# Kernel optimization log

Measured on AMD Instinct MI355X. Metric: run time of the kernel, lower is better.

Reference implementation:

```python
import jax, jax.numpy as jnp
import numpy as np

B, L, D, C, NL = 32, 512, 768, 97, 2  # batch, seq_len, hidden, class_nums, gat_layers


def setup_inputs() -> dict:
    key = jax.random.key(0)
    ks = jax.random.split(key, 16)

    def n(k, shape, scale=0.02):
        return jax.random.normal(k, shape, dtype=jnp.float32) * scale

    return dict(
        x=n(ks[0], (B, L, D), 1.0),                 # encoder output
        pos1=jnp.ones((B, L), jnp.float32),          # entity-1 position mask
        pos2=jnp.ones((B, L), jnp.float32),          # entity-2 position mask
        mask=jnp.ones((B, L), jnp.int32),            # attention mask (1 = keep)
        emb=n(ks[1], (C, D), 1.0),                   # relation label embedding table
        rel_w=n(ks[2], (D, D)), rel_b=jnp.zeros((D,), jnp.float32),
        # per-layer, per-RA (axis1: 0=ra1, 1=ra2) parameters
        qw=n(ks[3], (NL, 2, D, D)), qb=jnp.zeros((NL, 2, D), jnp.float32),
        kw=n(ks[4], (NL, 2, D, D)), kb=jnp.zeros((NL, 2, D), jnp.float32),
        vw=n(ks[5], (NL, 2, D, D)), vb=jnp.zeros((NL, 2, D), jnp.float32),
        sw=n(ks[6], (NL, 2, 2 * D)), sb=jnp.zeros((NL, 2), jnp.float32),   # score: Linear(2d,1)
        gw=n(ks[7], (NL, 2, 2 * D)), gb=jnp.zeros((NL, 2), jnp.float32),   # gate:  Linear(2d,1)
        fc1_w=n(ks[8], (3 * D, D)), fc1_b=jnp.zeros((D,), jnp.float32),
        fc2_w=n(ks[9], (D,)), fc2_b=jnp.zeros((), jnp.float32),
    )


def _relation_attention(p, x, qw, qb, kw, kb, vw, vb, sw, sb, gw, gb, mask):
    # p: (b, c, d) queries; x: (b, l, d) keys/values
    d = p.shape[-1]
    q = jnp.einsum('bcd,de->bce', p, qw) + qb          # (b, c, d)
    k = jnp.einsum('bld,de->ble', x, kw) + kb          # (b, l, d)
    # score = Linear(concat([q_i, k_j])) is separable: q@sw[:d] + k@sw[d:] + sb
    score = (q @ sw[:d])[:, :, None] + (k @ sw[d:])[:, None, :] + sb  # (b, c, l)
    if mask is not None:
        score = jnp.where(mask[:, None, :] == 0, jnp.float32(-1e9), score)
    attn = jax.nn.softmax(score, axis=2)
    v = jnp.einsum('bld,de->ble', x, vw) + vb          # (b, l, d)
    out = jnp.einsum('bcl,bld->bcd', attn, v) + p      # (b, c, d)
    # gate = sigmoid(Linear(concat([out, p]))), also separable
    g = jax.nn.sigmoid(out @ gw[:d] + p @ gw[d:] + gb)[..., None]
    return g * out + (1.0 - g) * p


def reference(x, pos1, pos2, mask, emb, rel_w, rel_b,
              qw, qb, kw, kb, vw, vb, sw, sb, gw, gb,
              fc1_w, fc1_b, fc2_w, fc2_b):
    b, d = x.shape[0], x.shape[-1]
    # p = relation(embedding(arange(C))) broadcast over batch
    p = emb @ rel_w + rel_b                            # (C, d)
    p = jnp.broadcast_to(p[None], (b,) + p.shape)      # (b, C, d)

    for li in range(qw.shape[0]):
        x = _relation_attention(x, p, qw[li, 0], qb[li, 0], kw[li, 0], kb[li, 0],
                                vw[li, 0], vb[li, 0], sw[li, 0], sb[li, 0],
                                gw[li, 0], gb[li, 0], None) + x
        p = _relation_attention(p, x, qw[li, 1], qb[li, 1], kw[li, 1], kb[li, 1],
                                vw[li, 1], vb[li, 1], sw[li, 1], sb[li, 1],
                                gw[li, 1], gb[li, 1], mask) + p

    def pool_avg(pos):
        return jnp.sum(x * pos[:, :, None], axis=1) / jnp.sum(pos, axis=1)[:, None]

    e1 = pool_avg(pos1)                                # (b, d)
    e2 = pool_avg(pos2)                                # (b, d)
    cshape = p.shape                                   # (b, C, d)
    pc = jnp.concatenate([p,
                          jnp.broadcast_to(e1[:, None, :], cshape),
                          jnp.broadcast_to(e2[:, None, :], cshape)], axis=2)  # (b, C, 3d)
    h = jnp.tanh(pc @ fc1_w + fc1_b)                   # (b, C, d)
    logits = jax.nn.sigmoid(h @ fc2_w + fc2_b)         # (b, C)
    pred = jnp.argmax(logits, axis=1)                  # (b,)
    return logits, pred
```

## Files before the change

### kernel.cpp

```cpp
#include <hip/hip_runtime.h>
#include <math.h>

#define NBLK 512
#define NTHR 256
static const int Bb = 32, Ls = 512, Dd = 768, Cc = 97;

struct KArgs {
    const float *x0, *pos1, *pos2;
    const int* mask;
    const float *emb, *rel_w, *rel_b, *kw, *vw, *vb, *sw, *gw, *gb;
    const float *fc1w, *fc1b, *fc2w, *fc2b;
    float* out;
    float *p0b, *pp, *sc, *avx1, *avx2, *av1, *av2, *aw1, *aw2, *S0, *S1, *xp1, *xp2, *geb;
    float *kvecs, *pdots, *g1buf, *xd, *gx1, *gx2, *awb;
    float* zbase;
    int zcount;
};

__device__ __forceinline__ float sigm(float x) { return 1.f / (1.f + expf(-x)); }

__device__ __forceinline__ float wred(float v) {
#pragma unroll
    for (int o = 32; o > 0; o >>= 1) v += __shfl_down(v, o, 64);
    return v;
}

__device__ __forceinline__ float blk_sum4(float v, float* shr) {
    v = wred(v);
    int t = threadIdx.x;
    if ((t & 63) == 0) shr[t >> 6] = v;
    __syncthreads();
    float r = shr[0] + shr[1] + shr[2] + shr[3];
    __syncthreads();
    return r;
}

__device__ void sgemm_dev(const float* __restrict__ A, const float* __restrict__ W,
                          const float* __restrict__ bias, float* __restrict__ C,
                          int M, int N, int K, int KC, int bx, int by, int bz,
                          float* As, float* Ws) {
    int tid = threadIdx.x;
    int tx = tid & 15, ty = tid >> 4;
    int bn = bx * 64, bm = by * 64;
    int kb = bz * KC;
    int arow = tid >> 2, akq = (tid & 3) << 2;
    int wrow = tid >> 4, wcol = (tid & 15) << 2;
    int gar = bm + arow;
    bool aval = gar < M;
    const float* Ap = A + (size_t)gar * K + kb + akq;
    const float* Wp = W + (size_t)(kb + wrow) * N + bn + wcol;
    float acc[4][4] = {{0.f}};
    float4 a4 = make_float4(0.f, 0.f, 0.f, 0.f);
    if (aval) a4 = *(const float4*)Ap;
    float4 w4 = *(const float4*)Wp;
    for (int k0 = 0; k0 < KC; k0 += 16) {
        __syncthreads();
        As[(akq + 0) * 64 + arow] = a4.x; As[(akq + 1) * 64 + arow] = a4.y;
        As[(akq + 2) * 64 + arow] = a4.z; As[(akq + 3) * 64 + arow] = a4.w;
        *(float4*)&Ws[wrow * 64 + wcol] = w4;
        __syncthreads();
        if (k0 + 16 < KC) {
            if (aval) a4 = *(const float4*)(Ap + k0 + 16);
            w4 = *(const float4*)(Wp + (size_t)(k0 + 16) * N);
        }
#pragma unroll
        for (int kk = 0; kk < 16; ++kk) {
            float4 a = *(const float4*)&As[kk * 64 + (ty << 2)];
            float4 b = *(const float4*)&Ws[kk * 64 + (tx << 2)];
            acc[0][0]+=a.x*b.x; acc[0][1]+=a.x*b.y; acc[0][2]+=a.x*b.z; acc[0][3]+=a.x*b.w;
            acc[1][0]+=a.y*b.x; acc[1][1]+=a.y*b.y; acc[1][2]+=a.y*b.z; acc[1][3]+=a.y*b.w;
            acc[2][0]+=a.z*b.x; acc[2][1]+=a.z*b.y; acc[2][2]+=a.z*b.z; acc[2][3]+=a.z*b.w;
            acc[3][0]+=a.w*b.x; acc[3][1]+=a.w*b.y; acc[3][2]+=a.w*b.z; acc[3][3]+=a.w*b.w;
        }
    }
    int gc = bn + (tx << 2);
    float4 bz4 = make_float4(0.f, 0.f, 0.f, 0.f);
    if (bz == 0 && bias) bz4 = *(const float4*)(bias + gc);
#pragma unroll
    for (int i = 0; i < 4; ++i) {
        int gr = bm + (ty << 2) + i;
        if (gr < M) {
            float* cp = C + (size_t)gr * N + gc;
            atomicAdd(cp + 0, acc[i][0] + bz4.x); atomicAdd(cp + 1, acc[i][1] + bz4.y);
            atomicAdd(cp + 2, acc[i][2] + bz4.z); atomicAdd(cp + 3, acc[i][3] + bz4.w);
        }
    }
}

__device__ void attn_gemv(const KArgs& a, int phase, int jlin,
                          float* xs, float* lw, float* shr) {
    int t = threadIdx.x;
    int jt = jlin % 3, b = (jlin / 3) % 32, kseg = jlin / 96;
    float v = -3.0e38f, g1 = 0.f;
    if (t < Cc) {
        if (phase == 0) v = a.pdots[t];
        else {
            g1 = sigm(a.pdots[194 + t] + a.sc[128 + b] + a.gb[1]);
            v = 2.f * a.pdots[97 + t] + g1 * a.sc[160 + b];
        }
    }
    if (phase == 1 && jt == 0 && kseg == 0 && t < Cc) a.g1buf[(size_t)b * Cc + t] = g1;
    float m = v;
#pragma unroll
    for (int o = 32; o > 0; o >>= 1) m = fmaxf(m, __shfl_down(m, o, 64));
    if ((t & 63) == 0) shr[t >> 6] = m;
    __syncthreads();
    m = fmaxf(fmaxf(shr[0], shr[1]), fmaxf(shr[2], shr[3]));
    __syncthreads();
    float e = (t < Cc) ? expf(v - m) : 0.f;
    float s = blk_sum4(e, shr);
    float wc = e / s;
    if (t < Cc) lw[t] = wc;
    float cg1 = blk_sum4(wc * g1, shr);
    float alpha = (phase == 0) ? 1.f : 2.f;
    if (t < 96) {
        int d = kseg * 96 + t;
        const float* pc = a.p0b + d;
        float acc2 = 0.f;
#pragma unroll 4
        for (int c = 0; c < Cc; ++c) acc2 += lw[c] * pc[(size_t)c * Dd];
        float val = alpha * acc2;
        if (phase == 1) val += cg1 * a.av1[(size_t)b * Dd + d];
        xs[t] = val;
    }
    __syncthreads();
    const float* W = a.vw + (size_t)(phase == 0 ? 0 : 2) * Dd * Dd;
    const float* bias = a.vb + (phase == 0 ? 0 : 2) * Dd;
    float* outp = (phase == 0) ? a.avx1 : a.avx2;
    int j = jt * 256 + t;
    float acc = (kseg == 0) ? bias[j] : 0.f;
    const float* wp = W + (size_t)(kseg * 96) * Dd + j;
#pragma unroll 8
    for (int dd = 0; dd < 96; ++dd) acc += xs[dd] * wp[(size_t)dd * Dd];
    atomicAdd(&outp[(size_t)b * Dd + j], acc);
    const float* da[4]; const float* db[4]; int nd; float* dout;
    if (phase == 0) {
        da[0]=a.gw;          db[0]=nullptr;
        da[1]=a.kvecs+Dd;    db[1]=nullptr;
        da[2]=a.gw+3072;     db[2]=a.gw+3840;
        da[3]=a.kvecs+3*Dd;  db[3]=nullptr;
        nd = 4; dout = a.sc;
    } else {
        da[0]=a.gw+3072;     db[0]=nullptr;
        da[1]=a.kvecs+3*Dd;  db[1]=nullptr;
        nd = 2; dout = a.sc + 224;
    }
    for (int vv = 0; vv < nd; ++vv) {
        float wv = da[vv][j] + (db[vv] ? db[vv][j] : 0.f);
        float p = blk_sum4(acc * wv, shr);
        if (t == 0) atomicAdd(&dout[vv * 32 + b], p);
    }
}

__device__ void mm_dev(const KArgs& a, int jlin, const float* S, float gamma,
                       const float* avA, const float* coefA, float multA,
                       const float* avB, const float* coefB, float multB,
                       const float* W, const float* bias, float* outp,
                       int ndots, const float* d0a, const float* d0b,
                       const float* d1a, const float* d2a, const float* d2b,
                       float* dout, float* xs, float* shr) {
    int t = threadIdx.x;
    int jt = jlin % 3, b = (jlin / 3) % 32, kseg = jlin / 96;
    if (t < 96) {
        int d = kseg * 96 + t;
        float v = gamma * S[(size_t)b * Dd + d];
        if (avA) v += multA * coefA[b] * avA[(size_t)b * Dd + d];
        if (avB) v += multB * coefB[b] * avB[(size_t)b * Dd + d];
        xs[t] = v;
    }
    __syncthreads();
    int j = jt * 256 + t;
    float acc = (kseg == 0 && bias) ? bias[j] : 0.f;
    const float* wp = W + (size_t)(kseg * 96) * Dd + j;
#pragma unroll 8
    for (int dd = 0; dd < 96; ++dd) acc += xs[dd] * wp[(size_t)dd * Dd];
    atomicAdd(&outp[(size_t)b * Dd + j], acc);
    if (ndots > 0) {
        float wv = d0a[j] + (d0b ? d0b[j] : 0.f);
        float p = blk_sum4(acc * wv, shr);
        if (t == 0) atomicAdd(&dout[b], p);
    }
    if (ndots > 1) {
        float p = blk_sum4(acc * d1a[j], shr);
        if (t == 0) atomicAdd(&dout[32 + b], p);
    }
    if (ndots > 2) {
        float wv = d2a[j] + (d2b ? d2b[j] : 0.f);
        float p = blk_sum4(acc * wv, shr);
        if (t == 0) atomicAdd(&dout[64 + b], p);
    }
}

__device__ void ge_dev(const KArgs& a, int jlin, float* xs, float* xs2) {
    int t = threadIdx.x;
    int jt = jlin % 3, b = (jlin / 3) % 32, kseg = jlin / 96;
    if (t < 96) {
        int d = kseg * 96 + t;
        float a1 = a.avx1[(size_t)b * Dd + d], a2 = a.avx2[(size_t)b * Dd + d];
        xs[t]  = (4.f * a.xp1[(size_t)b * Dd + d] + 2.f * a.sc[448 + b] * a1 + a.sc[480 + b] * a2) * a.sc[576 + b];
        xs2[t] = (4.f * a.xp2[(size_t)b * Dd + d] + 2.f * a.sc[512 + b] * a1 + a.sc[544 + b] * a2) * a.sc[608 + b];
    }
    __syncthreads();
    int j = jt * 256 + t;
    float a1 = 0.f, a2 = 0.f;
    const float* w1 = a.fc1w + (size_t)(Dd + kseg * 96) * Dd + j;
    const float* w2 = a.fc1w + (size_t)(2 * Dd + kseg * 96) * Dd + j;
#pragma unroll 8
    for (int dd = 0; dd < 96; ++dd) {
        a1 += xs[dd] * w1[(size_t)dd * Dd];
        a2 += xs2[dd] * w2[(size_t)dd * Dd];
    }
    float res = a1 + a2 + (kseg == 0 ? a.fc1b[j] : 0.f);
    atomicAdd(&a.geb[(size_t)b * Dd + j], res);
}

__device__ void aw_dual_dev(const KArgs& a, int jlin, float* xs, float* xs2) {
    int t = threadIdx.x;
    int jt = jlin % 3, b = (jlin / 3) % 32, kseg = jlin / 96;
    if (t < 96) {
        int d = kseg * 96 + t;
        xs[t]  = a.av1[(size_t)b * Dd + d];
        xs2[t] = a.av2[(size_t)b * Dd + d];
    }
    __syncthreads();
    int j = jt * 256 + t;
    float a1 = 0.f, a2 = 0.f;
    const float* wp = a.fc1w + (size_t)(kseg * 96) * Dd + j;
#pragma unroll 8
    for (int dd = 0; dd < 96; ++dd) {
        float w = wp[(size_t)dd * Dd];
        a1 += xs[dd] * w;
        a2 += xs2[dd] * w;
    }
    atomicAdd(&a.aw1[(size_t)b * Dd + j], a1);
    atomicAdd(&a.aw2[(size_t)b * Dd + j], a2);
}

__device__ void softgate_dev(const KArgs& a, int phase, int b, float* shr) {
    int t = threadIdx.x;
    float ks[2], ga[2] = {0.f, 0.f}, gb2[2] = {0.f, 0.f};
#pragma unroll
    for (int i = 0; i < 2; ++i) {
        int l = t + (i << 8);
        size_t r = (size_t)b * Ls + l;
        float4 x = *(const float4*)(a.xd + r * 4);
        if (phase == 0) {
            float g = sigm(x.x + a.sc[b] + a.gb[0]);
            a.gx1[r] = g;
            ga[i] = g;
            ks[i] = 2.f * x.y + g * a.sc[32 + b];
        } else {
            float gp = a.gx1[r];
            float g = sigm(2.f * x.z + gp * a.sc[64 + b] + a.sc[224 + b] + a.gb[2]);
            a.gx2[r] = g;
            ga[i] = gp; gb2[i] = g;
            ks[i] = 4.f * x.w + 2.f * gp * a.sc[96 + b] + g * a.sc[256 + b];
        }
        if (a.mask[r] == 0) ks[i] = -1e9f;
    }
    float mx = fmaxf(ks[0], ks[1]);
#pragma unroll
    for (int o = 32; o > 0; o >>= 1) mx = fmaxf(mx, __shfl_down(mx, o, 64));
    if ((t & 63) == 0) shr[t >> 6] = mx;
    __syncthreads();
    mx = fmaxf(fmaxf(shr[0], shr[1]), fmaxf(shr[2], shr[3]));
    __syncthreads();
    float e0 = expf(ks[0] - mx), e1 = expf(ks[1] - mx);
    float s = blk_sum4(e0 + e1, shr);
    float inv = 1.f / s;
    float w0 = e0 * inv, w1 = e1 * inv;
    a.awb[(size_t)b * Ls + t] = w0;
    a.awb[(size_t)b * Ls + t + 256] = w1;
    float ca = blk_sum4(w0 * ga[0] + w1 * ga[1], shr);
    if (phase == 0) {
        if (t == 0) a.sc[320 + b] = ca;
    } else {
        if (t == 0) a.sc[352 + b] = ca;
        float cb = blk_sum4(w0 * gb2[0] + w1 * gb2[1], shr);
        if (t == 0) a.sc[384 + b] = cb;
        float q1a = a.pos1[(size_t)b * Ls + t], q1b = a.pos1[(size_t)b * Ls + t + 256];
        float q2a = a.pos2[(size_t)b * Ls + t], q2b = a.pos2[(size_t)b * Ls + t + 256];
        float s1 = blk_sum4(q1a + q1b, shr);
        float s2 = blk_sum4(q2a + q2b, shr);
        float c11 = blk_sum4(q1a * ga[0] + q1b * ga[1], shr);
        float c12 = blk_sum4(q1a * gb2[0] + q1b * gb2[1], shr);
        float c21 = blk_sum4(q2a * ga[0] + q2b * ga[1], shr);
        float c22 = blk_sum4(q2a * gb2[0] + q2b * gb2[1], shr);
        if (t == 0) {
            a.sc[448 + b] = c11; a.sc[480 + b] = c12;
            a.sc[512 + b] = c21; a.sc[544 + b] = c22;
            a.sc[576 + b] = 1.f / s1; a.sc[608 + b] = 1.f / s2;
        }
    }
}

__device__ void passX_dev(const KArgs& a, int blk, float* S, bool dopos) {
    int t = threadIdx.x;
    if (t >= 192) return;
    int b = blk >> 4, seg = blk & 15, l0 = seg * 32;
    int d4 = t << 2;
    const float* xb = a.x0 + ((size_t)b * Ls + l0) * Dd + d4;
    const float* wb = a.awb + (size_t)b * Ls + l0;
    float4 as = make_float4(0.f,0.f,0.f,0.f);
    float4 a1 = make_float4(0.f,0.f,0.f,0.f);
    float4 a2 = make_float4(0.f,0.f,0.f,0.f);
    for (int l = 0; l < 32; ++l) {
        float4 xv = *(const float4*)(xb + (size_t)l * Dd);
        float wv = wb[l];
        as.x += wv*xv.x; as.y += wv*xv.y; as.z += wv*xv.z; as.w += wv*xv.w;
        if (dopos) {
            float q1 = a.pos1[(size_t)b * Ls + l0 + l], q2 = a.pos2[(size_t)b * Ls + l0 + l];
            a1.x += q1*xv.x; a1.y += q1*xv.y; a1.z += q1*xv.z; a1.w += q1*xv.w;
            a2.x += q2*xv.x; a2.y += q2*xv.y; a2.z += q2*xv.z; a2.w += q2*xv.w;
        }
    }
    float* ds = S + (size_t)b * Dd + d4;
    atomicAdd(ds+0, as.x); atomicAdd(ds+1, as.y); atomicAdd(ds+2, as.z); atomicAdd(ds+3, as.w);
    if (dopos) {
        float* d1 = a.xp1 + (size_t)b * Dd + d4;
        float* d2 = a.xp2 + (size_t)b * Dd + d4;
        atomicAdd(d1+0, a1.x); atomicAdd(d1+1, a1.y); atomicAdd(d1+2, a1.z); atomicAdd(d1+3, a1.w);
        atomicAdd(d2+0, a2.x); atomicAdd(d2+1, a2.y); atomicAdd(d2+2, a2.z); atomicAdd(d2+3, a2.w);
    }
}

__global__ __launch_bounds__(NTHR) void k_zero_kvec(KArgs a) {
    int blk = blockIdx.x, t = threadIdx.x;
    int wv_ = t >> 6, lane = t & 63;
    for (size_t i = (size_t)blk * NTHR + t; i < (size_t)a.zcount; i += (size_t)NBLK * NTHR)
        a.zbase[i] = 0.f;
    int g = blk * 4 + wv_;
    for (int rep = 0; rep < 2; ++rep) {
        int dot = g + rep * 2048;
        if (dot < 3072) {
            int idx = dot / Dd, d = dot - idx * Dd;
            const float* row = a.kw + ((size_t)idx * Dd + d) * Dd;
            const float* swk = a.sw + (size_t)idx * 2 * Dd + Dd;
            float sA = 0.f;
            for (int j = lane; j < Dd; j += 64) sA += row[j] * swk[j];
            sA = wred(sA);
            if (lane == 0) a.kvecs[dot] = sA;
        }
    }
}

__global__ __launch_bounds__(NTHR) void k_gemm1(KArgs a) {
    __shared__ float As[1024], Ws[1024];
    int blk = blockIdx.x;
    sgemm_dev(a.emb, a.rel_w, a.rel_b, a.p0b, Cc, Dd, Dd, 96,
              blk % 12, (blk / 12) % 2, blk / 24, As, Ws);
}

__global__ __launch_bounds__(NTHR) void k_prep2(KArgs a) {
    __shared__ float As[1024], Ws[1024];
    int blk = blockIdx.x, t = threadIdx.x;
    int wv_ = t >> 6, lane = t & 63;
    if (blk < 96) {
        sgemm_dev(a.p0b, a.fc1w, nullptr, a.pp, Cc, Dd, Dd, 192,
                  blk % 12, (blk / 12) % 2, blk / 24, As, Ws);
    } else if (blk < 128) {
        int g2 = (blk - 96) * 4 + wv_;
        for (int k = 0; k < 4; ++k) {
            int j = g2 + k * 128;
            if (k == 3) { if (g2 >= 4) break; j = 384 + g2; }
            if (j >= 388) continue;
            int vv = j / Cc, r = j - vv * Cc;
            const float* va; const float* vb2 = nullptr;
            if (vv == 0) va = a.kvecs;
            else if (vv == 1) va = a.kvecs + 2 * Dd;
            else if (vv == 2) { va = a.gw + 1536; vb2 = a.gw + 2304; }
            else { va = a.gw + 4608; vb2 = a.gw + 5376; }
            const float* row = a.p0b + (size_t)r * Dd;
            float sA = 0.f;
            for (int jj = lane; jj < Dd; jj += 64)
                sA += row[jj] * (va[jj] + (vb2 ? vb2[jj] : 0.f));
            sA = wred(sA);
            if (lane == 0) a.pdots[j] = sA;
        }
    } else {
        float4 gs0[3], k1r[3], gs2[3], k3r[3];
#pragma unroll
        for (int k = 0; k < 3; ++k) {
            int d = (lane << 2) + k * 256;
            float4 ga = *(const float4*)(a.gw + d);
            float4 gbv = *(const float4*)(a.gw + 768 + d);
            gs0[k] = make_float4(ga.x+gbv.x, ga.y+gbv.y, ga.z+gbv.z, ga.w+gbv.w);
            k1r[k] = *(const float4*)(a.kvecs + 768 + d);
            float4 g2a = *(const float4*)(a.gw + 3072 + d);
            float4 g2b = *(const float4*)(a.gw + 3840 + d);
            gs2[k] = make_float4(g2a.x+g2b.x, g2a.y+g2b.y, g2a.z+g2b.z, g2a.w+g2b.w);
            k3r[k] = *(const float4*)(a.kvecs + 2304 + d);
        }
        int gwv = (blk - 128) * 4 + wv_;
        for (int r = gwv; r < Bb * Ls; r += 1536) {
            const float* xr = a.x0 + (size_t)r * Dd;
            float s0 = 0.f, s1 = 0.f, s2 = 0.f, s3 = 0.f;
#pragma unroll
            for (int k = 0; k < 3; ++k) {
                float4 xv = *(const float4*)(xr + (lane << 2) + k * 256);
                s0 += xv.x*gs0[k].x + xv.y*gs0[k].y + xv.z*gs0[k].z + xv.w*gs0[k].w;
                s1 += xv.x*k1r[k].x + xv.y*k1r[k].y + xv.z*k1r[k].z + xv.w*k1r[k].w;
                s2 += xv.x*gs2[k].x + xv.y*gs2[k].y + xv.z*gs2[k].z + xv.w*gs2[k].w;
                s3 += xv.x*k3r[k].x + xv.y*k3r[k].y + xv.z*k3r[k].z + xv.w*k3r[k].w;
            }
            s0 = wred(s0); s1 = wred(s1); s2 = wred(s2); s3 = wred(s3);
            if (lane == 0) {
                float4 o4 = make_float4(s0, s1, s2, s3);
                *(float4*)(a.xd + (size_t)r * 4) = o4;
            }
        }
    }
}

__global__ __launch_bounds__(NTHR) void k_attn(KArgs a, int phase) {
    __shared__ float xs[96], lw[128], shr[16];
    attn_gemv(a, phase, blockIdx.x, xs, lw, shr);
}

__global__ __launch_bounds__(NTHR) void k_softgate(KArgs a, int phase) {
    __shared__ float shr[16];
    softgate_dev(a, phase, blockIdx.x, shr);
}

__global__ __launch_bounds__(NTHR) void k_passX0(KArgs a) {
    passX_dev(a, blockIdx.x, a.S0, true);
}

__global__ __launch_bounds__(NTHR) void k_mm0(KArgs a) {
    __shared__ float xs[96], shr[16];
    mm_dev(a, blockIdx.x, a.S0, 2.f, a.avx1, a.sc + 320, 1.f, nullptr, nullptr, 0.f,
           a.vw + (size_t)1 * Dd * Dd, a.vb + Dd, a.av1,
           3, a.gw + 1536, nullptr, a.kvecs + 2 * Dd, a.gw + 4608, a.gw + 5376,
           a.sc + 128, xs, shr);
}

__global__ __launch_bounds__(NTHR) void k_passX1ge(KArgs a) {
    __shared__ float xs[96], xs2[96];
    int blk = blockIdx.x;
    if (blk < 512) passX_dev(a, blk, a.S1, false);
    else ge_dev(a, blk - 512, xs, xs2);
}

__global__ __launch_bounds__(NTHR) void k_mm1(KArgs a) {
    __shared__ float xs[96], shr[16];
    mm_dev(a, blockIdx.x, a.S1, 4.f, a.avx1, a.sc + 352, 2.f, a.avx2, a.sc + 384, 1.f,
           a.vw + (size_t)3 * Dd * Dd, a.vb + 3 * Dd, a.av2,
           1, a.gw + 4608, nullptr, nullptr, nullptr, nullptr,
           a.sc + 288, xs, shr);
}

__global__ __launch_bounds__(NTHR) void k_awdual(KArgs a) {
    __shared__ float xs[96], xs2[96];
    aw_dual_dev(a, blockIdx.x, xs, xs2);
}

__global__ __launch_bounds__(NTHR) void k_logits(KArgs a) {
    __shared__ float shr[16];
    int blk = blockIdx.x, t = threadIdx.x;
    for (int r = blk; r < Bb * Cc; r += NBLK) {
        int b = r / Cc, c = r - b * Cc;
        float g1 = a.g1buf[r];
        float g2 = sigm(2.f * a.pdots[291 + c] + g1 * a.sc[192 + b] + a.sc[288 + b] + a.gb[3]);
        float ssum = 0.f;
#pragma unroll
        for (int sseg = 0; sseg < 3; ++sseg) {
            int d = t + sseg * 256;
            float h = tanhf(4.f * a.pp[(size_t)c * Dd + d]
                          + 2.f * g1 * a.aw1[(size_t)b * Dd + d]
                          + g2 * a.aw2[(size_t)b * Dd + d]
                          + a.geb[(size_t)b * Dd + d]);
            ssum += h * a.fc2w[d];
        }
        float tt = blk_sum4(ssum, shr);
        if (t == 0) a.out[r] = sigm(tt + a.fc2b[0]);
    }
}

__global__ void k_argmax(KArgs a) {
    int t = threadIdx.x;
    if (t < Bb) {
        const float* row = a.out + (size_t)t * Cc;
        float best = row[0];
        int bi = 0;
        for (int c = 1; c < Cc; ++c) {
            float v = row[c];
            if (v > best) { best = v; bi = c; }
        }
        a.out[Bb * Cc + t] = (float)bi;
    }
}

extern "C" void kernel_launch(void* const* d_in, const int* in_sizes, int n_in,
                              void* d_out, int out_size, void* d_ws, size_t ws_size,
                              hipStream_t stream) {
    KArgs ka;
    ka.x0    = (const float*)d_in[0];
    ka.pos1  = (const float*)d_in[1];
    ka.pos2  = (const float*)d_in[2];
    ka.mask  = (const int*)d_in[3];
    ka.emb   = (const float*)d_in[4];
    ka.rel_w = (const float*)d_in[5];
    ka.rel_b = (const float*)d_in[6];
    ka.kw    = (const float*)d_in[9];
    ka.vw    = (const float*)d_in[11];
    ka.vb    = (const float*)d_in[12];
    ka.sw    = (const float*)d_in[13];
    ka.gw    = (const float*)d_in[15];
    ka.gb    = (const float*)d_in[16];
    ka.fc1w  = (const float*)d_in[17];
    ka.fc1b  = (const float*)d_in[18];
    ka.fc2w  = (const float*)d_in[19];
    ka.fc2b  = (const float*)d_in[20];
    ka.out   = (float*)d_out;

    float* ws = (float*)d_ws;
    size_t off = 0;
    const size_t PD = (size_t)Cc * Dd;
    const size_t BD = (size_t)Bb * Dd;
    ka.p0b  = ws + off; off += PD;
    ka.pp   = ws + off; off += PD;
    ka.sc   = ws + off; off += 640;
    ka.avx1 = ws + off; off += BD;
    ka.avx2 = ws + off; off += BD;
    ka.av1  = ws + off; off += BD;
    ka.av2  = ws + off; off += BD;
    ka.aw1  = ws + off; off += BD;
    ka.aw2  = ws + off; off += BD;
    ka.S0   = ws + off; off += BD;
    ka.S1   = ws + off; off += BD;
    ka.xp1  = ws + off; off += BD;
    ka.xp2  = ws + off; off += BD;
    ka.geb  = ws + off; off += BD;
    ka.zbase = ws;
    ka.zcount = (int)off;
    ka.kvecs = ws + off; off += (size_t)4 * Dd;
    ka.pdots = ws + off; off += 388;
    ka.g1buf = ws + off; off += (size_t)Bb * Cc;
    ka.xd    = ws + off; off += (size_t)Bb * Ls * 4;
    ka.gx1   = ws + off; off += (size_t)Bb * Ls;
    ka.gx2   = ws + off; off += (size_t)Bb * Ls;
    ka.awb   = ws + off; off += (size_t)Bb * Ls;

    k_zero_kvec<<<NBLK, NTHR, 0, stream>>>(ka);
    k_gemm1<<<192, NTHR, 0, stream>>>(ka);
    k_prep2<<<NBLK, NTHR, 0, stream>>>(ka);
    k_attn<<<768, NTHR, 0, stream>>>(ka, 0);
    k_softgate<<<32, NTHR, 0, stream>>>(ka, 0);
    k_passX0<<<NBLK, NTHR, 0, stream>>>(ka);
    k_mm0<<<768, NTHR, 0, stream>>>(ka);
    k_attn<<<768, NTHR, 0, stream>>>(ka, 1);
    k_softgate<<<32, NTHR, 0, stream>>>(ka, 1);
    k_passX1ge<<<1280, NTHR, 0, stream>>>(ka);
    k_mm1<<<768, NTHR, 0, stream>>>(ka);
    k_awdual<<<768, NTHR, 0, stream>>>(ka);
    k_logits<<<NBLK, NTHR, 0, stream>>>(ka);
    k_argmax<<<1, 64, 0, stream>>>(ka);
}
```

Baseline: 339.4 us.

## Fuse all stages into one persistent kernel with software grid barriers

Replaces fourteen separate kernel launches with an init kernel plus a single persistent 256-block kernel whose stages are separated by an atomic-counter grid barrier. It also regroups the work: the rel_w GEMM now overlaps with the x-projection dot products instead of running in its own launch. This removes per-launch overhead and the idle tails between kernels. In exchange, each stage runs on fewer blocks via grid-stride loops, the barriers spin, and correctness depends on all 256 blocks being co-resident.

```diff
diff --git a/kernel.cpp b/kernel.cpp
--- a/kernel.cpp
+++ b/kernel.cpp
@@ -1,7 +1,7 @@
 #include <hip/hip_runtime.h>
 #include <math.h>
 
-#define NBLK 512
+#define GRID 256
 #define NTHR 256
 static const int Bb = 32, Ls = 512, Dd = 768, Cc = 97;
 
@@ -13,6 +13,7 @@
     float* out;
     float *p0b, *pp, *sc, *avx1, *avx2, *av1, *av2, *aw1, *aw2, *S0, *S1, *xp1, *xp2, *geb;
     float *kvecs, *pdots, *g1buf, *xd, *gx1, *gx2, *awb;
+    int* bar;
     float* zbase;
     int zcount;
 };
@@ -33,6 +34,23 @@
     float r = shr[0] + shr[1] + shr[2] + shr[3];
     __syncthreads();
     return r;
+}
+
+__device__ void gbar(int* bar, int epoch) {
+    __syncthreads();
+    if (threadIdx.x == 0) {
+        __threadfence();
+        int old = atomicAdd(&bar[0], 1);
+        if (old == GRID - 1) {
+            bar[0] = 0;
+            __threadfence();
+            atomicExch(&bar[1], epoch);
+        } else {
+            while (atomicAdd(&bar[1], 0) < epoch) __builtin_amdgcn_s_sleep(1);
+        }
+        __threadfence();
+    }
+    __syncthreads();
 }
 
 __device__ void sgemm_dev(const float* __restrict__ A, const float* __restrict__ W,
@@ -85,6 +103,7 @@
             atomicAdd(cp + 2, acc[i][2] + bz4.z); atomicAdd(cp + 3, acc[i][3] + bz4.w);
         }
     }
+    __syncthreads();
 }
 
 __device__ void attn_gemv(const KArgs& a, int phase, int jlin,
@@ -150,6 +169,7 @@
         float p = blk_sum4(acc * wv, shr);
         if (t == 0) atomicAdd(&dout[vv * 32 + b], p);
     }
+    __syncthreads();
 }
 
 __device__ void mm_dev(const KArgs& a, int jlin, const float* S, float gamma,
@@ -189,6 +209,7 @@
         float p = blk_sum4(acc * wv, shr);
         if (t == 0) atomicAdd(&dout[64 + b], p);
     }
+    __syncthreads();
 }
 
 __device__ void ge_dev(const KArgs& a, int jlin, float* xs, float* xs2) {
@@ -212,6 +233,7 @@
     }
     float res = a1 + a2 + (kseg == 0 ? a.fc1b[j] : 0.f);
     atomicAdd(&a.geb[(size_t)b * Dd + j], res);
+    __syncthreads();
 }
 
 __device__ void aw_dual_dev(const KArgs& a, int jlin, float* xs, float* xs2) {
@@ -234,6 +256,7 @@
     }
     atomicAdd(&a.aw1[(size_t)b * Dd + j], a1);
     atomicAdd(&a.aw2[(size_t)b * Dd + j], a2);
+    __syncthreads();
 }
 
 __device__ void softgate_dev(const KArgs& a, int phase, int b, float* shr) {
@@ -292,6 +315,7 @@
             a.sc[576 + b] = 1.f / s1; a.sc[608 + b] = 1.f / s2;
         }
     }
+    __syncthreads();
 }
 
 __device__ void passX_dev(const KArgs& a, int blk, float* S, bool dopos) {
@@ -324,46 +348,77 @@
     }
 }
 
-__global__ __launch_bounds__(NTHR) void k_zero_kvec(KArgs a) {
+__global__ __launch_bounds__(NTHR) void k_init(KArgs a) {
+    size_t i = (size_t)blockIdx.x * NTHR + threadIdx.x;
+    for (; i < (size_t)a.zcount; i += (size_t)512 * NTHR) a.zbase[i] = 0.f;
+    if (blockIdx.x == 0 && threadIdx.x < 16) a.bar[threadIdx.x] = 0;
+}
+
+__global__ __launch_bounds__(NTHR) void mega(KArgs a) {
+    __shared__ float As[1024], Ws[1024];
+    __shared__ float xs[96], xs2[96];
+    __shared__ float lw[128];
+    __shared__ float shr[16];
     int blk = blockIdx.x, t = threadIdx.x;
     int wv_ = t >> 6, lane = t & 63;
-    for (size_t i = (size_t)blk * NTHR + t; i < (size_t)a.zcount; i += (size_t)NBLK * NTHR)
-        a.zbase[i] = 0.f;
-    int g = blk * 4 + wv_;
-    for (int rep = 0; rep < 2; ++rep) {
-        int dot = g + rep * 2048;
-        if (dot < 3072) {
-            int idx = dot / Dd, d = dot - idx * Dd;
-            const float* row = a.kw + ((size_t)idx * Dd + d) * Dd;
-            const float* swk = a.sw + (size_t)idx * 2 * Dd + Dd;
-            float sA = 0.f;
-            for (int j = lane; j < Dd; j += 64) sA += row[j] * swk[j];
-            sA = wred(sA);
-            if (lane == 0) a.kvecs[dot] = sA;
-        }
-    }
-}
-
-__global__ __launch_bounds__(NTHR) void k_gemm1(KArgs a) {
-    __shared__ float As[1024], Ws[1024];
-    int blk = blockIdx.x;
-    sgemm_dev(a.emb, a.rel_w, a.rel_b, a.p0b, Cc, Dd, Dd, 96,
-              blk % 12, (blk / 12) % 2, blk / 24, As, Ws);
-}
-
-__global__ __launch_bounds__(NTHR) void k_prep2(KArgs a) {
-    __shared__ float As[1024], Ws[1024];
-    int blk = blockIdx.x, t = threadIdx.x;
-    int wv_ = t >> 6, lane = t & 63;
+    int wgid = blk * 4 + wv_;
+
+    for (int dot = wgid; dot < 3072; dot += 1024) {
+        int idx = dot / Dd, d = dot - idx * Dd;
+        const float* row = a.kw + ((size_t)idx * Dd + d) * Dd;
+        const float* swk = a.sw + (size_t)idx * 2 * Dd + Dd;
+        float sA = 0.f;
+        for (int j = lane; j < Dd; j += 64) sA += row[j] * swk[j];
+        sA = wred(sA);
+        if (lane == 0) a.kvecs[dot] = sA;
+    }
+    gbar(a.bar, 1);
+
+    if (blk < 96) {
+        for (int job = blk; job < 192; job += 96)
+            sgemm_dev(a.emb, a.rel_w, a.rel_b, a.p0b, Cc, Dd, Dd, 96,
+                      job % 12, (job / 12) % 2, job / 24, As, Ws);
+    } else {
+        float4 gs0[3], k1r[3], gs2[3], k3r[3];
+#pragma unroll
+        for (int k = 0; k < 3; ++k) {
+            int d = (lane << 2) + k * 256;
+            float4 ga = *(const float4*)(a.gw + d);
+            float4 gbv = *(const float4*)(a.gw + 768 + d);
+            gs0[k] = make_float4(ga.x+gbv.x, ga.y+gbv.y, ga.z+gbv.z, ga.w+gbv.w);
+            k1r[k] = *(const float4*)(a.kvecs + 768 + d);
+            float4 g2a = *(const float4*)(a.gw + 3072 + d);
+            float4 g2b = *(const float4*)(a.gw + 3840 + d);
+            gs2[k] = make_float4(g2a.x+g2b.x, g2a.y+g2b.y, g2a.z+g2b.z, g2a.w+g2b.w);
+            k3r[k] = *(const float4*)(a.kvecs + 2304 + d);
+        }
+        int wloc = (blk - 96) * 4 + wv_;
+        for (int r = wloc; r < Bb * Ls; r += 640) {
+            const float* xr = a.x0 + (size_t)r * Dd;
+            float s0 = 0.f, s1 = 0.f, s2 = 0.f, s3 = 0.f;
+#pragma unroll
+            for (int k = 0; k < 3; ++k) {
+                float4 xv = *(const float4*)(xr + (lane << 2) + k * 256);
+                s0 += xv.x*gs0[k].x + xv.y*gs0[k].y + xv.z*gs0[k].z + xv.w*gs0[k].w;
+                s1 += xv.x*k1r[k].x + xv.y*k1r[k].y + xv.z*k1r[k].z + xv.w*k1r[k].w;
+                s2 += xv.x*gs2[k].x + xv.y*gs2[k].y + xv.z*gs2[k].z + xv.w*gs2[k].w;
+                s3 += xv.x*k3r[k].x + xv.y*k3r[k].y + xv.z*k3r[k].z + xv.w*k3r[k].w;
+            }
+            s0 = wred(s0); s1 = wred(s1); s2 = wred(s2); s3 = wred(s3);
+            if (lane == 0) {
+                float4 o4 = make_float4(s0, s1, s2, s3);
+                *(float4*)(a.xd + (size_t)r * 4) = o4;
+            }
+        }
+    }
+    gbar(a.bar, 2);
+
     if (blk < 96) {
         sgemm_dev(a.p0b, a.fc1w, nullptr, a.pp, Cc, Dd, Dd, 192,
                   blk % 12, (blk / 12) % 2, blk / 24, As, Ws);
     } else if (blk < 128) {
-        int g2 = (blk - 96) * 4 + wv_;
-        for (int k = 0; k < 4; ++k) {
-            int j = g2 + k * 128;
-            if (k == 3) { if (g2 >= 4) break; j = 384 + g2; }
-            if (j >= 388) continue;
+        int wloc = (blk - 96) * 4 + wv_;
+        for (int j = wloc; j < 388; j += 128) {
             int vv = j / Cc, r = j - vv * Cc;
             const float* va; const float* vb2 = nullptr;
             if (vv == 0) va = a.kvecs;
@@ -377,87 +432,48 @@
             sA = wred(sA);
             if (lane == 0) a.pdots[j] = sA;
         }
-    } else {
-        float4 gs0[3], k1r[3], gs2[3], k3r[3];
-#pragma unroll
-        for (int k = 0; k < 3; ++k) {
-            int d = (lane << 2) + k * 256;
-            float4 ga = *(const float4*)(a.gw + d);
-            float4 gbv = *(const float4*)(a.gw + 768 + d);
-            gs0[k] = make_float4(ga.x+gbv.x, ga.y+gbv.y, ga.z+gbv.z, ga.w+gbv.w);
-            k1r[k] = *(const float4*)(a.kvecs + 768 + d);
-            float4 g2a = *(const float4*)(a.gw + 3072 + d);
-            float4 g2b = *(const float4*)(a.gw + 3840 + d);
-            gs2[k] = make_float4(g2a.x+g2b.x, g2a.y+g2b.y, g2a.z+g2b.z, g2a.w+g2b.w);
-            k3r[k] = *(const float4*)(a.kvecs + 2304 + d);
-        }
-        int gwv = (blk - 128) * 4 + wv_;
-        for (int r = gwv; r < Bb * Ls; r += 1536) {
-            const float* xr = a.x0 + (size_t)r * Dd;
-            float s0 = 0.f, s1 = 0.f, s2 = 0.f, s3 = 0.f;
-#pragma unroll
-            for (int k = 0; k < 3; ++k) {
-                float4 xv = *(const float4*)(xr + (lane << 2) + k * 256);
-                s0 += xv.x*gs0[k].x + xv.y*gs0[k].y + xv.z*gs0[k].z + xv.w*gs0[k].w;
-                s1 += xv.x*k1r[k].x + xv.y*k1r[k].y + xv.z*k1r[k].z + xv.w*k1r[k].w;
-                s2 += xv.x*gs2[k].x + xv.y*gs2[k].y + xv.z*gs2[k].z + xv.w*gs2[k].w;
-                s3 += xv.x*k3r[k].x + xv.y*k3r[k].y + xv.z*k3r[k].z + xv.w*k3r[k].w;
-            }
-            s0 = wred(s0); s1 = wred(s1); s2 = wred(s2); s3 = wred(s3);
-            if (lane == 0) {
-                float4 o4 = make_float4(s0, s1, s2, s3);
-                *(float4*)(a.xd + (size_t)r * 4) = o4;
-            }
-        }
-    }
-}
-
-__global__ __launch_bounds__(NTHR) void k_attn(KArgs a, int phase) {
-    __shared__ float xs[96], lw[128], shr[16];
-    attn_gemv(a, phase, blockIdx.x, xs, lw, shr);
-}
-
-__global__ __launch_bounds__(NTHR) void k_softgate(KArgs a, int phase) {
-    __shared__ float shr[16];
-    softgate_dev(a, phase, blockIdx.x, shr);
-}
-
-__global__ __launch_bounds__(NTHR) void k_passX0(KArgs a) {
-    passX_dev(a, blockIdx.x, a.S0, true);
-}
-
-__global__ __launch_bounds__(NTHR) void k_mm0(KArgs a) {
-    __shared__ float xs[96], shr[16];
-    mm_dev(a, blockIdx.x, a.S0, 2.f, a.avx1, a.sc + 320, 1.f, nullptr, nullptr, 0.f,
-           a.vw + (size_t)1 * Dd * Dd, a.vb + Dd, a.av1,
-           3, a.gw + 1536, nullptr, a.kvecs + 2 * Dd, a.gw + 4608, a.gw + 5376,
-           a.sc + 128, xs, shr);
-}
-
-__global__ __launch_bounds__(NTHR) void k_passX1ge(KArgs a) {
-    __shared__ float xs[96], xs2[96];
-    int blk = blockIdx.x;
-    if (blk < 512) passX_dev(a, blk, a.S1, false);
-    else ge_dev(a, blk - 512, xs, xs2);
-}
-
-__global__ __launch_bounds__(NTHR) void k_mm1(KArgs a) {
-    __shared__ float xs[96], shr[16];
-    mm_dev(a, blockIdx.x, a.S1, 4.f, a.avx1, a.sc + 352, 2.f, a.avx2, a.sc + 384, 1.f,
-           a.vw + (size_t)3 * Dd * Dd, a.vb + 3 * Dd, a.av2,
-           1, a.gw + 4608, nullptr, nullptr, nullptr, nullptr,
-           a.sc + 288, xs, shr);
-}
-
-__global__ __launch_bounds__(NTHR) void k_awdual(KArgs a) {
-    __shared__ float xs[96], xs2[96];
-    aw_dual_dev(a, blockIdx.x, xs, xs2);
-}
-
-__global__ __launch_bounds__(NTHR) void k_logits(KArgs a) {
-    __shared__ float shr[16];
-    int blk = blockIdx.x, t = threadIdx.x;
-    for (int r = blk; r < Bb * Cc; r += NBLK) {
+    }
+    gbar(a.bar, 3);
+
+    for (int job = blk; job < 768; job += GRID) attn_gemv(a, 0, job, xs, lw, shr);
+    gbar(a.bar, 4);
+
+    if (blk < 32) softgate_dev(a, 0, blk, shr);
+    gbar(a.bar, 5);
+
+    for (int job = blk; job < 512; job += GRID) passX_dev(a, job, a.S0, true);
+    gbar(a.bar, 6);
+
+    for (int job = blk; job < 768; job += GRID)
+        mm_dev(a, job, a.S0, 2.f, a.avx1, a.sc + 320, 1.f, nullptr, nullptr, 0.f,
+               a.vw + (size_t)1 * Dd * Dd, a.vb + Dd, a.av1,
+               3, a.gw + 1536, nullptr, a.kvecs + 2 * Dd, a.gw + 4608, a.gw + 5376,
+               a.sc + 128, xs, shr);
+    gbar(a.bar, 7);
+
+    for (int job = blk; job < 768; job += GRID) attn_gemv(a, 1, job, xs, lw, shr);
+    gbar(a.bar, 8);
+
+    if (blk < 32) softgate_dev(a, 1, blk, shr);
+    gbar(a.bar, 9);
+
+    for (int job = blk; job < 1280; job += GRID) {
+        if (job < 512) passX_dev(a, job, a.S1, false);
+        else ge_dev(a, job - 512, xs, xs2);
+    }
+    gbar(a.bar, 10);
+
+    for (int job = blk; job < 768; job += GRID)
+        mm_dev(a, job, a.S1, 4.f, a.avx1, a.sc + 352, 2.f, a.avx2, a.sc + 384, 1.f,
+               a.vw + (size_t)3 * Dd * Dd, a.vb + 3 * Dd, a.av2,
+               1, a.gw + 4608, nullptr, nullptr, nullptr, nullptr,
+               a.sc + 288, xs, shr);
+    gbar(a.bar, 11);
+
+    for (int job = blk; job < 768; job += GRID) aw_dual_dev(a, job, xs, xs2);
+    gbar(a.bar, 12);
+
+    for (int r = blk; r < Bb * Cc; r += GRID) {
         int b = r / Cc, c = r - b * Cc;
         float g1 = a.g1buf[r];
         float g2 = sigm(2.f * a.pdots[291 + c] + g1 * a.sc[192 + b] + a.sc[288 + b] + a.gb[3]);
@@ -474,11 +490,9 @@
         float tt = blk_sum4(ssum, shr);
         if (t == 0) a.out[r] = sigm(tt + a.fc2b[0]);
     }
-}
-
-__global__ void k_argmax(KArgs a) {
-    int t = threadIdx.x;
-    if (t < Bb) {
+    gbar(a.bar, 13);
+
+    if (blk == 0 && t < Bb) {
         const float* row = a.out + (size_t)t * Cc;
         float best = row[0];
         int bi = 0;
@@ -533,6 +547,7 @@
     ka.geb  = ws + off; off += BD;
     ka.zbase = ws;
     ka.zcount = (int)off;
+    ka.bar   = (int*)(ws + off); off += 16;
     ka.kvecs = ws + off; off += (size_t)4 * Dd;
     ka.pdots = ws + off; off += 388;
     ka.g1buf = ws + off; off += (size_t)Bb * Cc;
@@ -541,18 +556,6 @@
     ka.gx2   = ws + off; off += (size_t)Bb * Ls;
     ka.awb   = ws + off; off += (size_t)Bb * Ls;
 
-    k_zero_kvec<<<NBLK, NTHR, 0, stream>>>(ka);
-    k_gemm1<<<192, NTHR, 0, stream>>>(ka);
-    k_prep2<<<NBLK, NTHR, 0, stream>>>(ka);
-    k_attn<<<768, NTHR, 0, stream>>>(ka, 0);
-    k_softgate<<<32, NTHR, 0, stream>>>(ka, 0);
-    k_passX0<<<NBLK, NTHR, 0, stream>>>(ka);
-    k_mm0<<<768, NTHR, 0, stream>>>(ka);
-    k_attn<<<768, NTHR, 0, stream>>>(ka, 1);
-    k_softgate<<<32, NTHR, 0, stream>>>(ka, 1);
-    k_passX1ge<<<1280, NTHR, 0, stream>>>(ka);
-    k_mm1<<<768, NTHR, 0, stream>>>(ka);
-    k_awdual<<<768, NTHR, 0, stream>>>(ka);
-    k_logits<<<NBLK, NTHR, 0, stream>>>(ka);
-    k_argmax<<<1, 64, 0, stream>>>(ka);
-}
+    k_init<<<512, NTHR, 0, stream>>>(ka);
+    mega<<<GRID, NTHR, 0, stream>>>(ka);
+}
```

New measurement: 677.3 us. 2x slower.
